# Kernel optimization log

Hardware: AMD Instinct MI355X
Metric: run time of the kernel (lower is better)

The kernel has to match this reference:

```python
import jax, jax.numpy as jnp
import numpy as np

B, S, K, H, W = 64, 100, 4, 32, 32

def setup_inputs() -> dict:
    key = jax.random.key(0)
    k1, k2 = jax.random.split(key)
    output = jax.random.normal(k1, (B, S, K, H, W), dtype=jnp.float32)
    convdata = jax.random.normal(k2, (B, S, K, H, W), dtype=jnp.float32)
    return {"output": output, "convdata": convdata}

def reference(output, convdata):
    # Original: sum over 32x32 of mean(|convdata[:,:,3,i,j] - output[:,:,3,i,j]|) / 1024
    # Each (i,j) slice has identical size, so this equals a single mean of the
    # abs-diff over the whole [B, S, 32, 32] slice at channel 3.
    return jnp.mean(jnp.abs(convdata[:, :, 3] - output[:, :, 3]))
```

## Files before the change

kernel.cpp:

```cpp
#include <hip/hip_runtime.h>


#define RBLOCKS 1024
#define RTHREADS 256

__global__ __launch_bounds__(RTHREADS)
void absdiff_partial_kernel(const float4* __restrict__ outp,
                            const float4* __restrict__ conv,
                            float* __restrict__ partials,
                            int n4) {
    float acc = 0.0f;
    const int stride = gridDim.x * blockDim.x;
    for (int v = blockIdx.x * blockDim.x + threadIdx.x; v < n4; v += stride) {
        const int pair = v >> 8;
        const int within = v & 255;
        const size_t g = (size_t)pair * 1024 + 768 + (size_t)within;
        const float4 a = outp[g];
        const float4 b = conv[g];
        acc += fabsf(b.x - a.x) + fabsf(b.y - a.y)
             + fabsf(b.z - a.z) + fabsf(b.w - a.w);
    }
    #pragma unroll
    for (int off = 32; off > 0; off >>= 1)
        acc += __shfl_down(acc, off, 64);
    __shared__ float smem[RTHREADS / 64];
    const int lane = threadIdx.x & 63;
    const int wave = threadIdx.x >> 6;
    if (lane == 0) smem[wave] = acc;
    __syncthreads();
    if (threadIdx.x == 0) {
        float s = 0.0f;
        #pragma unroll
        for (int w = 0; w < RTHREADS / 64; ++w) s += smem[w];
        partials[blockIdx.x] = s;
    }
}

__global__ __launch_bounds__(RTHREADS)
void final_reduce_kernel(const float* __restrict__ partials,
                         float* __restrict__ out,
                         int n, float inv_total) {
    float acc = 0.0f;
    for (int i = threadIdx.x; i < n; i += RTHREADS) acc += partials[i];
    #pragma unroll
    for (int off = 32; off > 0; off >>= 1)
        acc += __shfl_down(acc, off, 64);
    __shared__ float smem[RTHREADS / 64];
    const int lane = threadIdx.x & 63;
    const int wave = threadIdx.x >> 6;
    if (lane == 0) smem[wave] = acc;
    __syncthreads();
    if (threadIdx.x == 0) {
        float s = 0.0f;
        #pragma unroll
        for (int w = 0; w < RTHREADS / 64; ++w) s += smem[w];
        out[0] = s * inv_total;
    }
}

extern "C" void kernel_launch(void* const* d_in, const int* in_sizes, int n_in,
                              void* d_out, int out_size, void* d_ws, size_t ws_size,
                              hipStream_t stream) {
    const float4* outp = (const float4*)d_in[0];
    const float4* conv = (const float4*)d_in[1];
    float* partials = (float*)d_ws;
    float* out = (float*)d_out;

    const int n_elems = 64 * 100 * 1024;
    const int n4 = n_elems / 4;
    const float inv_total = 1.0f / (float)n_elems;

    absdiff_partial_kernel<<<RBLOCKS, RTHREADS, 0, stream>>>(outp, conv, partials, n4);
    final_reduce_kernel<<<1, RTHREADS, 0, stream>>>(partials, out, RBLOCKS, inv_total);
}
```

Before: 180.8 us.

## Fuse partial and final reduction via atomicAdd with fixed per-block tiles

Replaces the grid-stride partial kernel plus single-block final reduce with one kernel in which each block handles four (batch, step) pairs and atomically adds its scaled sum into the output. All loads are issued up front for memory-level parallelism, and a memset zeroes the output first. This removes the second kernel launch and the workspace round trip. In exchange it adds 1600 atomics on one address and makes the float summation order nondeterministic.

New measurement: 191.0 us. 1.06x slower.

```diff
diff --git a/kernel.cpp b/kernel.cpp
--- a/kernel.cpp
+++ b/kernel.cpp
@@ -1,60 +1,49 @@
 #include <hip/hip_runtime.h>
 
 
-#define RBLOCKS 1024
-#define RTHREADS 256
+#define PAIRS_TOTAL 6400
+#define PAIRS_PER_BLOCK 4
+#define NBLOCKS (PAIRS_TOTAL / PAIRS_PER_BLOCK)
+#define NTHREADS 256
 
-__global__ __launch_bounds__(RTHREADS)
-void absdiff_partial_kernel(const float4* __restrict__ outp,
-                            const float4* __restrict__ conv,
-                            float* __restrict__ partials,
-                            int n4) {
+__global__ __launch_bounds__(NTHREADS)
+void absdiff_mean_fused_kernel(const float4* __restrict__ outp,
+                               const float4* __restrict__ conv,
+                               float* __restrict__ out,
+                               float inv_total) {
+    const int t = threadIdx.x;
+    const size_t base = (size_t)blockIdx.x * (PAIRS_PER_BLOCK * 1024) + 768 + t;
+
+    float4 a[PAIRS_PER_BLOCK], b[PAIRS_PER_BLOCK];
+    #pragma unroll
+    for (int c = 0; c < PAIRS_PER_BLOCK; ++c) {
+        const size_t g = base + (size_t)c * 1024;
+        a[c] = outp[g];
+        b[c] = conv[g];
+    }
+
     float acc = 0.0f;
-    const int stride = gridDim.x * blockDim.x;
-    for (int v = blockIdx.x * blockDim.x + threadIdx.x; v < n4; v += stride) {
-        const int pair = v >> 8;
-        const int within = v & 255;
-        const size_t g = (size_t)pair * 1024 + 768 + (size_t)within;
-        const float4 a = outp[g];
-        const float4 b = conv[g];
-        acc += fabsf(b.x - a.x) + fabsf(b.y - a.y)
-             + fabsf(b.z - a.z) + fabsf(b.w - a.w);
+    #pragma unroll
+    for (int c = 0; c < PAIRS_PER_BLOCK; ++c) {
+        acc += fabsf(b[c].x - a[c].x) + fabsf(b[c].y - a[c].y)
+             + fabsf(b[c].z - a[c].z) + fabsf(b[c].w - a[c].w);
     }
+
     #pragma unroll
     for (int off = 32; off > 0; off >>= 1)
         acc += __shfl_down(acc, off, 64);
-    __shared__ float smem[RTHREADS / 64];
-    const int lane = threadIdx.x & 63;
-    const int wave = threadIdx.x >> 6;
+
+    __shared__ float smem[NTHREADS / 64];
+    const int lane = t & 63;
+    const int wave = t >> 6;
     if (lane == 0) smem[wave] = acc;
     __syncthreads();
-    if (threadIdx.x == 0) {
+
+    if (t == 0) {
         float s = 0.0f;
         #pragma unroll
-        for (int w = 0; w < RTHREADS / 64; ++w) s += smem[w];
-        partials[blockIdx.x] = s;
-    }
-}
-
-__global__ __launch_bounds__(RTHREADS)
-void final_reduce_kernel(const float* __restrict__ partials,
-                         float* __restrict__ out,
-                         int n, float inv_total) {
-    float acc = 0.0f;
-    for (int i = threadIdx.x; i < n; i += RTHREADS) acc += partials[i];
-    #pragma unroll
-    for (int off = 32; off > 0; off >>= 1)
-        acc += __shfl_down(acc, off, 64);
-    __shared__ float smem[RTHREADS / 64];
-    const int lane = threadIdx.x & 63;
-    const int wave = threadIdx.x >> 6;
-    if (lane == 0) smem[wave] = acc;
-    __syncthreads();
-    if (threadIdx.x == 0) {
-        float s = 0.0f;
-        #pragma unroll
-        for (int w = 0; w < RTHREADS / 64; ++w) s += smem[w];
-        out[0] = s * inv_total;
+        for (int w = 0; w < NTHREADS / 64; ++w) s += smem[w];
+        atomicAdd(out, s * inv_total);
     }
 }
 
@@ -63,13 +52,10 @@
                               hipStream_t stream) {
     const float4* outp = (const float4*)d_in[0];
     const float4* conv = (const float4*)d_in[1];
-    float* partials = (float*)d_ws;
     float* out = (float*)d_out;
 
-    const int n_elems = 64 * 100 * 1024;
-    const int n4 = n_elems / 4;
-    const float inv_total = 1.0f / (float)n_elems;
+    const float inv_total = 1.0f / (float)(PAIRS_TOTAL * 1024);
 
-    absdiff_partial_kernel<<<RBLOCKS, RTHREADS, 0, stream>>>(outp, conv, partials, n4);
-    final_reduce_kernel<<<1, RTHREADS, 0, stream>>>(partials, out, RBLOCKS, inv_total);
+    hipMemsetAsync(out, 0, sizeof(float), stream);
+    absdiff_mean_fused_kernel<<<NBLOCKS, NTHREADS, 0, stream>>>(outp, conv, out, inv_total);
 }
```
